# Kernel tuning notes

Measured on AMD Instinct MI355X. Metric: run time of the kernel, lower is better.

## Reference

```python
import jax, jax.numpy as jnp
import numpy as np

L_SEQ = 32768
H_FEAT = 512
P_STATE = 256  # state_size // 2 (conj_sym)
LOG_DT_MIN, LOG_DT_MAX = np.log(1e-3), np.log(1e-1)


def setup_inputs() -> dict:
    key = jax.random.key(0)
    ks = jax.random.split(key, 7)
    input_sequence = jax.random.normal(ks[0], (L_SEQ, H_FEAT), dtype=jnp.float32)
    # eigenvalue real parts must be negative for stability (HiPPO-LegS-like)
    lambda_real = -jax.random.uniform(ks[1], (P_STATE,), minval=0.1, maxval=1.0, dtype=jnp.float32)
    lambda_imag = jax.random.normal(ks[2], (P_STATE,), dtype=jnp.float32) * float(np.pi)
    b = jax.random.normal(ks[3], (P_STATE, H_FEAT, 2), dtype=jnp.float32) / np.sqrt(H_FEAT)
    c = jax.random.normal(ks[4], (H_FEAT, P_STATE, 2), dtype=jnp.float32) / np.sqrt(P_STATE)
    d = jax.random.normal(ks[5], (H_FEAT,), dtype=jnp.float32)
    # log-timestep init in [log(1e-3), log(1e-1)] as in init_log_steps
    delta = (LOG_DT_MIN + jax.random.uniform(ks[6], (P_STATE, 1), dtype=jnp.float32)
             * (LOG_DT_MAX - LOG_DT_MIN))
    return {"input_sequence": input_sequence, "lambda_real": lambda_real,
            "lambda_imag": lambda_imag, "b": b, "c": c, "d": d, "delta": delta}


def _binop(e_i, e_j):
    A_i, b_i = e_i
    A_j, b_j = e_j
    return A_j * A_i, A_j * b_i + b_j


def reference(input_sequence, lambda_real, lambda_imag, b, c, d, delta):
    # assemble complex parameters (stored as real [..., 2])
    Lam = lambda_real + 1j * lambda_imag            # [P]
    B = b[..., 0] + 1j * b[..., 1]                  # [P, H]
    C = c[..., 0] + 1j * c[..., 1]                  # [H, P]
    step = jnp.exp(delta[:, 0])                     # step_rescale = 1.0
    # bilinear discretization
    BL = 1.0 / (1.0 - (step / 2.0) * Lam)
    Lam_bar = BL * (1.0 + (step / 2.0) * Lam)       # [P]
    B_bar = (BL * step)[:, None] * B                # [P, H]
    # input projection: Bu[l] = B_bar @ u[l]
    Bu = jnp.einsum('lh,ph->lp', input_sequence.astype(Lam_bar.dtype), B_bar)  # [L, P]
    L = input_sequence.shape[0]
    Lam_el = jnp.broadcast_to(Lam_bar, (L, Lam_bar.shape[0]))
    _, xs = jax.lax.associative_scan(_binop, (Lam_el, Bu))  # xs: [L, P] complex states
    # output projection (conj_sym => factor 2, real part)
    ys = 2.0 * jnp.einsum('lp,hp->lh', xs, C).real  # [L, H]
    return ys + d * input_sequence
```

## Files before the change

kernel.cpp:

```cpp
#include <hip/hip_runtime.h>
#include <cstddef>

#define L_SEQ 32768
#define H_FEAT 512
#define P_STATE 256
#define N2 512
#define CS 32
#define NCH (L_SEQ / CS)

typedef __bf16 bf16x8 __attribute__((ext_vector_type(8)));
typedef float f32x4 __attribute__((ext_vector_type(4)));

#define GLDS16(g, l) __builtin_amdgcn_global_load_lds( \
    (const __attribute__((address_space(1))) void*)(g), \
    (__attribute__((address_space(3))) void*)(l), 16, 0, 0)

__device__ __forceinline__ unsigned bf_rne(float x) {
    unsigned u = __float_as_uint(x);
    return (u + 0x7fffu + ((u >> 16) & 1u)) >> 16;
}
__device__ __forceinline__ float bf_f(unsigned bits) {
    return __uint_as_float(bits << 16);
}

__global__ __launch_bounds__(256) void param_kernel(
    const float* __restrict__ lr, const float* __restrict__ li,
    const float* __restrict__ b,  const float* __restrict__ c,
    const float* __restrict__ delta,
    ushort* __restrict__ W_hi, ushort* __restrict__ W_lo,
    ushort* __restrict__ C2_hi, ushort* __restrict__ C2_lo,
    float2* __restrict__ Abar)
{
    int tid = blockIdx.x * blockDim.x + threadIdx.x;

    {
        int p = tid >> 9;
        int h = tid & 511;
        float step = expf(delta[p]);
        float zr = 0.5f * step * lr[p];
        float zi = 0.5f * step * li[p];
        float dr = 1.0f - zr, di = -zi;
        float den = dr * dr + di * di;
        float blr = dr / den, bli = -di / den;
        float bbr = blr * step, bbi = bli * step;
        float b0 = b[((size_t)(p * H_FEAT + h)) * 2 + 0];
        float b1 = b[((size_t)(p * H_FEAT + h)) * 2 + 1];
        float vr = bbr * b0 - bbi * b1;
        float vi = bbr * b1 + bbi * b0;
        unsigned hr = bf_rne(vr), hl = bf_rne(vr - bf_f(hr));
        unsigned ir = bf_rne(vi), il = bf_rne(vi - bf_f(ir));
        size_t o0 = (size_t)(2 * p) * H_FEAT + h;
        size_t o1 = (size_t)(2 * p + 1) * H_FEAT + h;
        W_hi[o0] = (ushort)hr; W_lo[o0] = (ushort)hl;
        W_hi[o1] = (ushort)ir; W_lo[o1] = (ushort)il;
    }

    {
        int h2 = tid >> 8;
        int p2 = tid & 255;
        float c0 =  2.0f * c[((size_t)(h2 * P_STATE + p2)) * 2 + 0];
        float c1 = -2.0f * c[((size_t)(h2 * P_STATE + p2)) * 2 + 1];
        unsigned h0 = bf_rne(c0), l0 = bf_rne(c0 - bf_f(h0));
        unsigned h1 = bf_rne(c1), l1 = bf_rne(c1 - bf_f(h1));
        size_t o0 = (size_t)h2 * N2 + 2 * p2;
        C2_hi[o0] = (ushort)h0;     C2_lo[o0] = (ushort)l0;
        C2_hi[o0 + 1] = (ushort)h1; C2_lo[o0 + 1] = (ushort)l1;
    }

    if (tid < P_STATE) {
        int p = tid;
        float step = expf(delta[p]);
        float zr = 0.5f * step * lr[p];
        float zi = 0.5f * step * li[p];
        float dr = 1.0f - zr, di = -zi;
        float den = dr * dr + di * di;
        float blr = dr / den, bli = -di / den;
        float nr = 1.0f + zr, ni = zi;
        Abar[p] = make_float2(blr * nr - bli * ni, blr * ni + bli * nr);
    }
}

__global__ __launch_bounds__(256, 2) void gemm1(
    const float* __restrict__ A,
    const ushort* __restrict__ Bhi, const ushort* __restrict__ Blo,
    float* __restrict__ C)
{
    __shared__ ushort As_hi[128 * 32], As_lo[128 * 32];
    __shared__ ushort Bs_hi[256 * 32], Bs_lo[256 * 32];
    const int tid = threadIdx.x;
    const int ln = tid & 63, wv = tid >> 6;
    const int bm = blockIdx.y * 128, bn = blockIdx.x * 256;
    const int m = ln & 15, q = ln >> 4;
    const int wr = (wv >> 1) * 64, wc = (wv & 1) * 128;

    f32x4 acc[4][8] = {};

    for (int k0 = 0; k0 < 512; k0 += 32) {
#pragma unroll
        for (int s = 0; s < 8; s++) {
            int t = wv * 8 + s;
            int ch = t & 15;
            int row = ch * 16 + (ln >> 2);
            const ushort* src = (t < 16 ? Bhi : Blo)
                                + (size_t)(bn + row) * 512 + k0 + (ln & 3) * 8;
            ushort* dst = (t < 16 ? Bs_hi : Bs_lo) + ch * 512 + ln * 8;
            GLDS16(src, dst);
        }
#pragma unroll
        for (int r = 0; r < 4; r++) {
            int idx = tid + r * 256;
            int row = idx >> 3;
            int c4 = (idx & 7) << 2;
            const float4 v = *(const float4*)(A + (size_t)(bm + row) * 512 + k0 + c4);
            unsigned u0 = __float_as_uint(v.x), u1 = __float_as_uint(v.y);
            unsigned u2 = __float_as_uint(v.z), u3 = __float_as_uint(v.w);
            unsigned hi01 = (u0 >> 16) | (u1 & 0xffff0000u);
            unsigned hi23 = (u2 >> 16) | (u3 & 0xffff0000u);
            float d0 = v.x - __uint_as_float(u0 & 0xffff0000u);
            float d1 = v.y - __uint_as_float(u1 & 0xffff0000u);
            float d2 = v.z - __uint_as_float(u2 & 0xffff0000u);
            float d3 = v.w - __uint_as_float(u3 & 0xffff0000u);
            unsigned lo01 = (__float_as_uint(d0) >> 16) | (__float_as_uint(d1) & 0xffff0000u);
            unsigned lo23 = (__float_as_uint(d2) >> 16) | (__float_as_uint(d3) & 0xffff0000u);
            *(uint2*)(As_hi + row * 32 + c4) = make_uint2(hi01, hi23);
            *(uint2*)(As_lo + row * 32 + c4) = make_uint2(lo01, lo23);
        }
        __syncthreads();

        bf16x8 ah[4], al[4];
#pragma unroll
        for (int i = 0; i < 4; i++) {
            ah[i] = *(const bf16x8*)(As_hi + (wr + i * 16 + m) * 32 + q * 8);
            al[i] = *(const bf16x8*)(As_lo + (wr + i * 16 + m) * 32 + q * 8);
        }
#pragma unroll
        for (int j = 0; j < 8; j++) {
            bf16x8 bh = *(const bf16x8*)(Bs_hi + (wc + j * 16 + m) * 32 + q * 8);
            bf16x8 bl = *(const bf16x8*)(Bs_lo + (wc + j * 16 + m) * 32 + q * 8);
#pragma unroll
            for (int i = 0; i < 4; i++)
                acc[i][j] = __builtin_amdgcn_mfma_f32_16x16x32_bf16(ah[i], bh, acc[i][j], 0, 0, 0);
#pragma unroll
            for (int i = 0; i < 4; i++)
                acc[i][j] = __builtin_amdgcn_mfma_f32_16x16x32_bf16(al[i], bh, acc[i][j], 0, 0, 0);
#pragma unroll
            for (int i = 0; i < 4; i++)
                acc[i][j] = __builtin_amdgcn_mfma_f32_16x16x32_bf16(ah[i], bl, acc[i][j], 0, 0, 0);
        }
        __syncthreads();
    }

#pragma unroll
    for (int i = 0; i < 4; i++)
#pragma unroll
        for (int j = 0; j < 8; j++)
#pragma unroll
            for (int r = 0; r < 4; r++) {
                int row = bm + wr + i * 16 + q * 4 + r;
                int col = bn + wc + j * 16 + m;
                C[(size_t)row * 512 + col] = acc[i][j][r];
            }
}

__global__ __launch_bounds__(256, 2) void gemm2(
    const unsigned* __restrict__ Xp,
    const ushort* __restrict__ Bhi, const ushort* __restrict__ Blo,
    float* __restrict__ Cout, const float* __restrict__ U,
    const float* __restrict__ dvec)
{
    __shared__ ushort As_hi[128 * 32], As_lo[128 * 32];
    __shared__ ushort Bs_hi[256 * 32], Bs_lo[256 * 32];
    const int tid = threadIdx.x;
    const int ln = tid & 63, wv = tid >> 6;
    const int bm = blockIdx.y * 128, bn = blockIdx.x * 256;
    const int m = ln & 15, q = ln >> 4;
    const int wr = (wv >> 1) * 64, wc = (wv & 1) * 128;

    f32x4 acc[4][8] = {};

    for (int k0 = 0; k0 < 512; k0 += 32) {
#pragma unroll
        for (int s = 0; s < 8; s++) {
            int t = wv * 8 + s;
            int ch = t & 15;
            int row = ch * 16 + (ln >> 2);
            const ushort* src = (t < 16 ? Bhi : Blo)
                                + (size_t)(bn + row) * 512 + k0 + (ln & 3) * 8;
            ushort* dst = (t < 16 ? Bs_hi : Bs_lo) + ch * 512 + ln * 8;
            GLDS16(src, dst);
        }
#pragma unroll
        for (int r = 0; r < 4; r++) {
            int idx = tid + r * 256;
            int row = idx >> 3;
            int c4 = (idx & 7) << 2;
            const uint4 v = *(const uint4*)(Xp + (size_t)(bm + row) * 512 + k0 + c4);
            unsigned hi01 = (v.x >> 16) | (v.y & 0xffff0000u);
            unsigned hi23 = (v.z >> 16) | (v.w & 0xffff0000u);
            unsigned lo01 = (v.x & 0xffffu) | (v.y << 16);
            unsigned lo23 = (v.z & 0xffffu) | (v.w << 16);
            *(uint2*)(As_hi + row * 32 + c4) = make_uint2(hi01, hi23);
            *(uint2*)(As_lo + row * 32 + c4) = make_uint2(lo01, lo23);
        }
        __syncthreads();

        bf16x8 ah[4], al[4];
#pragma unroll
        for (int i = 0; i < 4; i++) {
            ah[i] = *(const bf16x8*)(As_hi + (wr + i * 16 + m) * 32 + q * 8);
            al[i] = *(const bf16x8*)(As_lo + (wr + i * 16 + m) * 32 + q * 8);
        }
#pragma unroll
        for (int j = 0; j < 8; j++) {
            bf16x8 bh = *(const bf16x8*)(Bs_hi + (wc + j * 16 + m) * 32 + q * 8);
            bf16x8 bl = *(const bf16x8*)(Bs_lo + (wc + j * 16 + m) * 32 + q * 8);
#pragma unroll
            for (int i = 0; i < 4; i++)
                acc[i][j] = __builtin_amdgcn_mfma_f32_16x16x32_bf16(ah[i], bh, acc[i][j], 0, 0, 0);
#pragma unroll
            for (int i = 0; i < 4; i++)
                acc[i][j] = __builtin_amdgcn_mfma_f32_16x16x32_bf16(al[i], bh, acc[i][j], 0, 0, 0);
#pragma unroll
            for (int i = 0; i < 4; i++)
                acc[i][j] = __builtin_amdgcn_mfma_f32_16x16x32_bf16(ah[i], bl, acc[i][j], 0, 0, 0);
        }
        __syncthreads();
    }

#pragma unroll
    for (int i = 0; i < 4; i++)
#pragma unroll
        for (int j = 0; j < 8; j++) {
            int col = bn + wc + j * 16 + m;
            float dv = dvec[col];
#pragma unroll
            for (int r = 0; r < 4; r++) {
                int row = bm + wr + i * 16 + q * 4 + r;
                Cout[(size_t)row * 512 + col] =
                    acc[i][j][r] + dv * U[(size_t)row * 512 + col];
            }
        }
}

__global__ __launch_bounds__(256) void scan_pass1(
    const float2* __restrict__ Bu, const float2* __restrict__ Abar,
    float2* __restrict__ ends)
{
    int tid = blockIdx.x * blockDim.x + threadIdx.x;
    int chunk = tid >> 8;
    int p = tid & 255;
    float2 A = Abar[p];
    float2 s = make_float2(0.f, 0.f);
    size_t base = (size_t)chunk * CS;
#pragma unroll 8
    for (int i = 0; i < CS; i++) {
        float2 u = Bu[(base + i) * P_STATE + p];
        float sr = fmaf(A.x, s.x, fmaf(-A.y, s.y, u.x));
        float si = fmaf(A.x, s.y, fmaf(A.y, s.x, u.y));
        s = make_float2(sr, si);
    }
    ends[(size_t)p * NCH + chunk] = s;
}

__global__ __launch_bounds__(1024) void scan_pass2(
    const float2* __restrict__ ends, const float2* __restrict__ Abar,
    float2* __restrict__ carries)
{
    __shared__ float2 sA[NCH];
    __shared__ float2 sB[NCH];
    int p = blockIdx.x;
    int t = threadIdx.x;

    float2 a = Abar[p];
#pragma unroll
    for (int i = 0; i < 5; i++) {
        float nr = a.x * a.x - a.y * a.y;
        float ni = 2.f * a.x * a.y;
        a = make_float2(nr, ni);
    }
    float2 A = a;
    float2 bv = ends[(size_t)p * NCH + t];
    sA[t] = A; sB[t] = bv;
    __syncthreads();

    for (int off = 1; off < NCH; off <<= 1) {
        float2 pa, pb;
        bool act = (t >= off);
        if (act) { pa = sA[t - off]; pb = sB[t - off]; }
        __syncthreads();
        if (act) {
            float2 nA = make_float2(A.x * pa.x - A.y * pa.y,
                                    A.x * pa.y + A.y * pa.x);
            float2 nB = make_float2(fmaf(A.x, pb.x, fmaf(-A.y, pb.y, bv.x)),
                                    fmaf(A.x, pb.y, fmaf(A.y, pb.x, bv.y)));
            A = nA; bv = nB;
            sA[t] = A; sB[t] = bv;
        }
        __syncthreads();
    }

    float2 carry = (t == 0) ? make_float2(0.f, 0.f) : sB[t - 1];
    carries[(size_t)p * NCH + t] = carry;
}

__global__ __launch_bounds__(256) void scan_pass3(
    uint2* __restrict__ Xp, const float2* __restrict__ Abar,
    const float2* __restrict__ carries)
{
    int tid = blockIdx.x * blockDim.x + threadIdx.x;
    int chunk = tid >> 8;
    int p = tid & 255;
    float2 A = Abar[p];
    float2 s = carries[(size_t)p * NCH + chunk];
    size_t base = (size_t)chunk * CS;
#pragma unroll 8
    for (int i = 0; i < CS; i++) {
        size_t off = (base + i) * P_STATE + p;
        uint2 ub = Xp[off];
        float ux = __uint_as_float(ub.x);
        float uy = __uint_as_float(ub.y);
        float sr = fmaf(A.x, s.x, fmaf(-A.y, s.y, ux));
        float si = fmaf(A.x, s.y, fmaf(A.y, s.x, uy));
        s = make_float2(sr, si);
        unsigned hr = bf_rne(sr);
        unsigned lr2 = __float_as_uint(sr - bf_f(hr)) >> 16;
        unsigned hi_ = bf_rne(si);
        unsigned li2 = __float_as_uint(si - bf_f(hi_)) >> 16;
        Xp[off] = make_uint2((hr << 16) | lr2, (hi_ << 16) | li2);
    }
}

extern "C" void kernel_launch(void* const* d_in, const int* in_sizes, int n_in,
                              void* d_out, int out_size, void* d_ws, size_t ws_size,
                              hipStream_t stream) {
    const float* u     = (const float*)d_in[0];
    const float* lr    = (const float*)d_in[1];
    const float* li    = (const float*)d_in[2];
    const float* b     = (const float*)d_in[3];
    const float* c     = (const float*)d_in[4];
    const float* dvec  = (const float*)d_in[5];
    const float* delta = (const float*)d_in[6];
    float* out = (float*)d_out;

    char* p = (char*)d_ws;
    float*  Bu      = (float*)p;   p += (size_t)L_SEQ * N2 * 4;
    float2* ends    = (float2*)p;  p += (size_t)P_STATE * NCH * 8;
    float2* carries = (float2*)p;  p += (size_t)P_STATE * NCH * 8;
    ushort* W_hi    = (ushort*)p;  p += (size_t)N2 * H_FEAT * 2;
    ushort* W_lo    = (ushort*)p;  p += (size_t)N2 * H_FEAT * 2;
    ushort* C2_hi   = (ushort*)p;  p += (size_t)H_FEAT * N2 * 2;
    ushort* C2_lo   = (ushort*)p;  p += (size_t)H_FEAT * N2 * 2;
    float2* Abar    = (float2*)p;  p += (size_t)P_STATE * 8;

    param_kernel<<<(P_STATE * H_FEAT) / 256, 256, 0, stream>>>(
        lr, li, b, c, delta, W_hi, W_lo, C2_hi, C2_lo, Abar);

    {
        dim3 grid(N2 / 256, L_SEQ / 128);
        gemm1<<<grid, 256, 0, stream>>>(u, W_hi, W_lo, Bu);
    }

    scan_pass1<<<(P_STATE * NCH) / 256, 256, 0, stream>>>(
        (const float2*)Bu, Abar, ends);
    scan_pass2<<<P_STATE, NCH, 0, stream>>>(ends, Abar, carries);
    scan_pass3<<<(P_STATE * NCH) / 256, 256, 0, stream>>>(
        (uint2*)Bu, Abar, carries);

    {
        dim3 grid(H_FEAT / 256, L_SEQ / 128);
        gemm2<<<grid, 256, 0, stream>>>((const unsigned*)Bu, C2_hi, C2_lo,
                                        out, u, dvec);
    }
}
```

Baseline: 253.7 us.

## Fuse three scan passes into one cooperative kernel keeping chunk inputs in registers

Replaces the three separate scan kernels with a single cooperative kernel that uses grid-wide syncs between the chunk-local pass, the cross-chunk carry scan, and the final fixup. Each thread loads its 32 chunk elements into registers once and reuses them in the final pass, so the second full read of Bu is avoided and two launches are dropped. The ends/carries layout is transposed to chunk-major. In exchange, the kernel holds 64 extra registers per thread at 1024 threads per block, needs all 256 blocks co-resident for the grid sync, and adds the cost of the grid barriers.

Result: slower. 531.3 us (+109.4%).

```diff
diff --git a/kernel.cpp b/kernel.cpp
--- a/kernel.cpp
+++ b/kernel.cpp
@@ -1,5 +1,8 @@
 #include <hip/hip_runtime.h>
+#include <hip/hip_cooperative_groups.h>
 #include <cstddef>
+
+namespace cg = cooperative_groups;
 
 #define L_SEQ 32768
 #define H_FEAT 512
@@ -242,91 +245,85 @@
         }
 }
 
-__global__ __launch_bounds__(256) void scan_pass1(
-    const float2* __restrict__ Bu, const float2* __restrict__ Abar,
-    float2* __restrict__ ends)
+__global__ __launch_bounds__(1024, 4) void scan_coop(
+    uint2* Bu, const float2* __restrict__ Abar,
+    float2* __restrict__ ends, float2* __restrict__ carries)
 {
-    int tid = blockIdx.x * blockDim.x + threadIdx.x;
-    int chunk = tid >> 8;
-    int p = tid & 255;
-    float2 A = Abar[p];
-    float2 s = make_float2(0.f, 0.f);
-    size_t base = (size_t)chunk * CS;
-#pragma unroll 8
-    for (int i = 0; i < CS; i++) {
-        float2 u = Bu[(base + i) * P_STATE + p];
-        float sr = fmaf(A.x, s.x, fmaf(-A.y, s.y, u.x));
-        float si = fmaf(A.x, s.y, fmaf(A.y, s.x, u.y));
-        s = make_float2(sr, si);
-    }
-    ends[(size_t)p * NCH + chunk] = s;
-}
-
-__global__ __launch_bounds__(1024) void scan_pass2(
-    const float2* __restrict__ ends, const float2* __restrict__ Abar,
-    float2* __restrict__ carries)
-{
-    __shared__ float2 sA[NCH];
-    __shared__ float2 sB[NCH];
-    int p = blockIdx.x;
-    int t = threadIdx.x;
-
-    float2 a = Abar[p];
-#pragma unroll
-    for (int i = 0; i < 5; i++) {
-        float nr = a.x * a.x - a.y * a.y;
-        float ni = 2.f * a.x * a.y;
-        a = make_float2(nr, ni);
-    }
-    float2 A = a;
-    float2 bv = ends[(size_t)p * NCH + t];
-    sA[t] = A; sB[t] = bv;
-    __syncthreads();
-
-    for (int off = 1; off < NCH; off <<= 1) {
-        float2 pa, pb;
-        bool act = (t >= off);
-        if (act) { pa = sA[t - off]; pb = sB[t - off]; }
-        __syncthreads();
-        if (act) {
-            float2 nA = make_float2(A.x * pa.x - A.y * pa.y,
-                                    A.x * pa.y + A.y * pa.x);
-            float2 nB = make_float2(fmaf(A.x, pb.x, fmaf(-A.y, pb.y, bv.x)),
-                                    fmaf(A.x, pb.y, fmaf(A.y, pb.x, bv.y)));
-            A = nA; bv = nB;
-            sA[t] = A; sB[t] = bv;
-        }
-        __syncthreads();
-    }
-
-    float2 carry = (t == 0) ? make_float2(0.f, 0.f) : sB[t - 1];
-    carries[(size_t)p * NCH + t] = carry;
-}
-
-__global__ __launch_bounds__(256) void scan_pass3(
-    uint2* __restrict__ Xp, const float2* __restrict__ Abar,
-    const float2* __restrict__ carries)
-{
-    int tid = blockIdx.x * blockDim.x + threadIdx.x;
-    int chunk = tid >> 8;
-    int p = tid & 255;
-    float2 A = Abar[p];
-    float2 s = carries[(size_t)p * NCH + chunk];
-    size_t base = (size_t)chunk * CS;
-#pragma unroll 8
-    for (int i = 0; i < CS; i++) {
-        size_t off = (base + i) * P_STATE + p;
-        uint2 ub = Xp[off];
-        float ux = __uint_as_float(ub.x);
-        float uy = __uint_as_float(ub.y);
-        float sr = fmaf(A.x, s.x, fmaf(-A.y, s.y, ux));
-        float si = fmaf(A.x, s.y, fmaf(A.y, s.x, uy));
-        s = make_float2(sr, si);
-        unsigned hr = bf_rne(sr);
-        unsigned lr2 = __float_as_uint(sr - bf_f(hr)) >> 16;
-        unsigned hi_ = bf_rne(si);
-        unsigned li2 = __float_as_uint(si - bf_f(hi_)) >> 16;
-        Xp[off] = make_uint2((hr << 16) | lr2, (hi_ << 16) | li2);
+    cg::grid_group grid = cg::this_grid();
+    const int tid = blockIdx.x * 1024 + threadIdx.x;
+    const int chunk = tid >> 8;
+    const int p = tid & 255;
+    const float2 A = Abar[p];
+
+    uint2 vals[CS];
+    const size_t base = (size_t)chunk * CS * P_STATE + p;
+#pragma unroll
+    for (int i = 0; i < CS; i++) vals[i] = Bu[base + (size_t)i * P_STATE];
+
+    {
+        float2 s = make_float2(0.f, 0.f);
+#pragma unroll
+        for (int i = 0; i < CS; i++) {
+            float ux = __uint_as_float(vals[i].x);
+            float uy = __uint_as_float(vals[i].y);
+            float sr = fmaf(A.x, s.x, fmaf(-A.y, s.y, ux));
+            float si = fmaf(A.x, s.y, fmaf(A.y, s.x, uy));
+            s = make_float2(sr, si);
+        }
+        ends[(size_t)chunk * P_STATE + p] = s;
+    }
+    __threadfence();
+    grid.sync();
+
+    {
+        __shared__ float2 sA[NCH], sB[NCH];
+        const int pp = blockIdx.x;
+        const int t = threadIdx.x;
+        float2 a = Abar[pp];
+#pragma unroll
+        for (int i = 0; i < 5; i++)
+            a = make_float2(a.x * a.x - a.y * a.y, 2.f * a.x * a.y);
+        float2 aggA = a;
+        float2 aggB = ends[(size_t)t * P_STATE + pp];
+        sA[t] = aggA; sB[t] = aggB;
+        __syncthreads();
+        for (int off = 1; off < NCH; off <<= 1) {
+            float2 pa, pb;
+            bool act = (t >= off);
+            if (act) { pa = sA[t - off]; pb = sB[t - off]; }
+            __syncthreads();
+            if (act) {
+                float2 nA = make_float2(aggA.x * pa.x - aggA.y * pa.y,
+                                        aggA.x * pa.y + aggA.y * pa.x);
+                float2 nB = make_float2(fmaf(aggA.x, pb.x, fmaf(-aggA.y, pb.y, aggB.x)),
+                                        fmaf(aggA.x, pb.y, fmaf(aggA.y, pb.x, aggB.y)));
+                aggA = nA; aggB = nB;
+                sA[t] = aggA; sB[t] = aggB;
+            }
+            __syncthreads();
+        }
+        float2 carry = (t == 0) ? make_float2(0.f, 0.f) : sB[t - 1];
+        carries[(size_t)t * P_STATE + pp] = carry;
+    }
+    __threadfence();
+    grid.sync();
+
+    {
+        float2 s = carries[(size_t)chunk * P_STATE + p];
+#pragma unroll
+        for (int i = 0; i < CS; i++) {
+            float ux = __uint_as_float(vals[i].x);
+            float uy = __uint_as_float(vals[i].y);
+            float sr = fmaf(A.x, s.x, fmaf(-A.y, s.y, ux));
+            float si = fmaf(A.x, s.y, fmaf(A.y, s.x, uy));
+            s = make_float2(sr, si);
+            unsigned hr = bf_rne(sr);
+            unsigned lr2 = __float_as_uint(sr - bf_f(hr)) >> 16;
+            unsigned hi_ = bf_rne(si);
+            unsigned li2 = __float_as_uint(si - bf_f(hi_)) >> 16;
+            Bu[base + (size_t)i * P_STATE] =
+                make_uint2((hr << 16) | lr2, (hi_ << 16) | li2);
+        }
     }
 }
 
@@ -360,11 +357,13 @@
         gemm1<<<grid, 256, 0, stream>>>(u, W_hi, W_lo, Bu);
     }
 
-    scan_pass1<<<(P_STATE * NCH) / 256, 256, 0, stream>>>(
-        (const float2*)Bu, Abar, ends);
-    scan_pass2<<<P_STATE, NCH, 0, stream>>>(ends, Abar, carries);
-    scan_pass3<<<(P_STATE * NCH) / 256, 256, 0, stream>>>(
-        (uint2*)Bu, Abar, carries);
+    {
+        uint2* BuIO = (uint2*)Bu;
+        void* args[] = { (void*)&BuIO, (void*)&Abar,
+                         (void*)&ends, (void*)&carries };
+        hipLaunchCooperativeKernel((const void*)scan_coop, dim3(256),
+                                   dim3(1024), args, 0, stream);
+    }
 
     {
         dim3 grid(H_FEAT / 256, L_SEQ / 128);
```
